# Optimization experiments

Measured on AMD Instinct MI355X. Metric: run time of the kernel, lower is better.

Reference implementation:

```python
import jax, jax.numpy as jnp
import numpy as np
from jax import lax

# CRF hyperparameters (init_kwargs)
MAX_ITER = 10
POS_W, POS_X_STD, POS_Y_STD = 3.0, 3.0, 3.0
BI_W, BI_X_STD, BI_Y_STD = 10.0, 80.0, 80.0
BI_R_STD, BI_G_STD, BI_B_STD = 13.0, 13.0, 13.0


def setup_inputs() -> dict:
    key = jax.random.key(0)
    k1, k2 = jax.random.split(key)
    U = jax.random.normal(k1, (1, 21, 96, 96), dtype=jnp.float32)      # unary energies
    I = jax.random.uniform(k2, (1, 3, 96, 96), dtype=jnp.float32) * 255.0  # RGB image 0..255
    return {"U": U, "I": I}


def _gauss1d(std):
    r = int(3.0 * std)
    x = jnp.arange(-r, r + 1, dtype=jnp.float32)
    return jnp.exp(-0.5 * (x / std) ** 2), r


def _spatial_raw(x, ky, kx, ry, rx):
    # x: [M, 1, H, W]; unnormalized separable Gaussian filter
    x = lax.conv_general_dilated(x, ky.reshape(1, 1, -1, 1), (1, 1), [(ry, ry), (0, 0)],
                                 dimension_numbers=("NCHW", "OIHW", "NCHW"))
    x = lax.conv_general_dilated(x, kx.reshape(1, 1, 1, -1), (1, 1), [(0, 0), (rx, rx)],
                                 dimension_numbers=("NCHW", "OIHW", "NCHW"))
    return x


def reference(U, I):
    B, L, H, W = U.shape
    N = H * W
    ky, ry = _gauss1d(POS_Y_STD)
    kx, rx = _gauss1d(POS_X_STD)

    # symmetric normalization for the spatial kernel: 1/sqrt(k * 1)
    nsp = lax.rsqrt(_spatial_raw(jnp.ones((1, 1, H, W), jnp.float32), ky, kx, ry, rx))  # [1,1,H,W]

    # bilateral kernel K[b, i, j] = exp(-0.5 ||f_i - f_j||^2) over 5-d features
    yy, xx = jnp.meshgrid(jnp.arange(H, dtype=jnp.float32), jnp.arange(W, dtype=jnp.float32), indexing="ij")
    pos = jnp.stack([xx.ravel() / BI_X_STD, yy.ravel() / BI_Y_STD], axis=-1)  # [N, 2]
    rgb_std = jnp.array([BI_R_STD, BI_G_STD, BI_B_STD], jnp.float32)
    col = I.reshape(B, 3, N).transpose(0, 2, 1) / rgb_std                     # [B, N, 3]
    feats = jnp.concatenate([jnp.broadcast_to(pos[None], (B, N, 2)), col], axis=-1)  # [B, N, 5]
    sq = jnp.sum(feats * feats, axis=-1)                                      # [B, N]
    D = sq[:, :, None] + sq[:, None, :] - 2.0 * jnp.einsum("bnf,bmf->bnm", feats, feats)
    K = jnp.exp(-0.5 * jnp.maximum(D, 0.0))                                   # [B, N, N]
    nbi = lax.rsqrt(jnp.sum(K, axis=-1, keepdims=True))                       # [B, N, 1]

    Q0 = jax.nn.softmax(-U, axis=1)

    def step(Q, _):
        Qf = Q.reshape(B * L, 1, H, W)
        sp_msg = POS_W * (nsp * _spatial_raw(nsp * Qf, ky, kx, ry, rx)).reshape(B, L, H, W)
        Qflat = Q.transpose(0, 2, 3, 1).reshape(B, N, L)
        bi = nbi * jnp.einsum("bnm,bml->bnl", K, nbi * Qflat)
        bi_msg = BI_W * bi.reshape(B, H, W, L).transpose(0, 3, 1, 2)
        # Potts compatibility (negative identity): agreeing mass raises the logit
        Qn = jax.nn.softmax(-U + sp_msg + bi_msg, axis=1)
        return Qn, None

    Q, _ = lax.scan(step, Q0, None, length=MAX_ITER)
    return Q
```

## Files before the change

### kernel.cpp

```cpp
#include <hip/hip_runtime.h>
#include <hip/hip_bf16.h>
#include <stddef.h>

#define HH 96
#define WW 96
#define NPIX 9216
#define LBL 21
#define LPAD 32
#define RAD 9
#define N_ITER 10
#define POS_W_C 3.0f
#define BI_W_C 10.0f
#define INV_XY (1.0f/80.0f)
#define INV_RGB (1.0f/13.0f)

#define JCH 16
#define JC (NPIX / JCH)
#define JTOT (NPIX / 32)
#define ITILE 64
#define NITB (NPIX / ITILE)
#define NSPB (LBL * 24)
#define KSPLIT 8
#define PSTR 24
#define QHALF (JTOT * 64 * 8)

typedef __bf16 bf16x8 __attribute__((ext_vector_type(8)));
typedef float  f32x4  __attribute__((ext_vector_type(4)));

__device__ const float GK[2 * RAD + 1] = {
    0.01110900f, 0.02856548f, 0.06572886f, 0.13533528f, 0.24935220f,
    0.41111229f, 0.60653066f, 0.80073740f, 0.94595947f, 1.00000000f,
    0.94595947f, 0.80073740f, 0.60653066f, 0.41111229f, 0.24935220f,
    0.13533528f, 0.06572886f, 0.02856548f, 0.01110900f
};

__device__ __forceinline__ unsigned short f2bf(float f) {
    unsigned u = __float_as_uint(f);
    unsigned r = (u + 0x7fffu + ((u >> 16) & 1u)) >> 16;
    return (unsigned short)r;
}
__device__ __forceinline__ float bf2f(unsigned short s) {
    return __uint_as_float(((unsigned)s) << 16);
}
__device__ __forceinline__ unsigned pk2bf(float a, float b) {
    __hip_bfloat162 h = __float22bfloat162_rn(make_float2(a, b));
    return *(unsigned*)&h;
}
__device__ __forceinline__ size_t qtidx(int p, int l) {
    size_t half = (l >> 4) ? (size_t)QHALF : 0;
    return half + ((((p >> 5) * 64 + ((p >> 3) & 3) * 16 + (l & 15)) << 3) + (p & 7));
}

__global__ void k_prep(const float* __restrict__ I,
                       float* __restrict__ fx, float* __restrict__ fy,
                       float* __restrict__ fr, float* __restrict__ fg,
                       float* __restrict__ fb, float* __restrict__ S,
                       float* __restrict__ nsp) {
    int n = blockIdx.x * 256 + threadIdx.x;
    if (n >= NPIX) return;
    int y = n / WW, x = n % WW;
    float vx = (float)x * INV_XY;
    float vy = (float)y * INV_XY;
    float vr = I[n] * INV_RGB;
    float vg = I[NPIX + n] * INV_RGB;
    float vb = I[2 * NPIX + n] * INV_RGB;
    fx[n] = vx; fy[n] = vy; fr[n] = vr; fg[n] = vg; fb[n] = vb;
    S[n] = -0.5f * (vx*vx + vy*vy + vr*vr + vg*vg + vb*vb);
    float sy = 0.f, sx = 0.f;
    #pragma unroll
    for (int d = -RAD; d <= RAD; ++d) {
        float g = GK[d + RAD];
        if ((unsigned)(y + d) < HH) sy += g;
        if ((unsigned)(x + d) < WW) sx += g;
    }
    nsp[n] = rsqrtf(sy * sx);
}

template <bool STORE>
__global__ void __launch_bounds__(256)
k_K(const float* __restrict__ fx, const float* __restrict__ fy,
    const float* __restrict__ fr, const float* __restrict__ fg,
    const float* __restrict__ fb, const float* __restrict__ S,
    float* __restrict__ RS, unsigned short* __restrict__ K) {
    int it = blockIdx.x >> 3;
    int part = blockIdx.x & 7;
    int tid = threadIdx.x;
    int m = tid & 15;
    int g = tid >> 4;
    int khs = g & 3;
    int ts = g >> 2;
    int i = it * 16 + m;
    float hx = fx[i], hy = fy[i], hr = fr[i], hg = fg[i], hb = fb[i];
    float ci = S[i];
    unsigned short* Kb = K + (size_t)it * JTOT * 512;
    float sum = 0.f;
    for (int pass = 0; pass < JTOT / (4 * KSPLIT); ++pass) {
        int jtile = part * (JTOT / KSPLIT) + pass * 4 + ts;
        int j = jtile * 32 + khs * 8;
        float4 x0 = *(const float4*)(fx + j), x1 = *(const float4*)(fx + j + 4);
        float4 y0 = *(const float4*)(fy + j), y1 = *(const float4*)(fy + j + 4);
        float4 r0 = *(const float4*)(fr + j), r1 = *(const float4*)(fr + j + 4);
        float4 g0 = *(const float4*)(fg + j), g1 = *(const float4*)(fg + j + 4);
        float4 b0 = *(const float4*)(fb + j), b1 = *(const float4*)(fb + j + 4);
        float4 s0 = *(const float4*)(S + j),  s1 = *(const float4*)(S + j + 4);
        float k0 = __expf(ci + s0.x + hx*x0.x + hy*y0.x + hr*r0.x + hg*g0.x + hb*b0.x);
        float k1 = __expf(ci + s0.y + hx*x0.y + hy*y0.y + hr*r0.y + hg*g0.y + hb*b0.y);
        float k2 = __expf(ci + s0.z + hx*x0.z + hy*y0.z + hr*r0.z + hg*g0.z + hb*b0.z);
        float k3 = __expf(ci + s0.w + hx*x0.w + hy*y0.w + hr*r0.w + hg*g0.w + hb*b0.w);
        float k4 = __expf(ci + s1.x + hx*x1.x + hy*y1.x + hr*r1.x + hg*g1.x + hb*b1.x);
        float k5 = __expf(ci + s1.y + hx*x1.y + hy*y1.y + hr*r1.y + hg*g1.y + hb*b1.y);
        float k6 = __expf(ci + s1.z + hx*x1.z + hy*y1.z + hr*r1.z + hg*g1.z + hb*b1.z);
        float k7 = __expf(ci + s1.w + hx*x1.w + hy*y1.w + hr*r1.w + hg*g1.w + hb*b1.w);
        sum += ((k0 + k1) + (k2 + k3)) + ((k4 + k5) + (k6 + k7));
        if (STORE) {
            uint4 u;
            u.x = pk2bf(k0, k1);
            u.y = pk2bf(k2, k3);
            u.z = pk2bf(k4, k5);
            u.w = pk2bf(k6, k7);
            *(uint4*)(Kb + (size_t)jtile * 512 + (tid & 63) * 8) = u;
        }
    }
    __shared__ float red[16][17];
    red[g][m] = sum;
    __syncthreads();
    if (tid < 16) {
        float tot = 0.f;
        #pragma unroll
        for (int q = 0; q < 16; ++q) tot += red[q][tid];
        RS[part * NPIX + it * 16 + tid] = tot;
    }
}

__global__ void k_q0(const float* __restrict__ U, const float* __restrict__ RS,
                     const float* __restrict__ nsp,
                     float* __restrict__ nbi, float* __restrict__ A,
                     unsigned short* __restrict__ Qt0, unsigned short* __restrict__ Qt1) {
    int n = blockIdx.x * 256 + threadIdx.x;
    if (n >= NPIX) return;
    float rs = 0.f;
    #pragma unroll
    for (int q = 0; q < KSPLIT; ++q) rs += RS[q * NPIX + n];
    float nb = rsqrtf(rs);
    nbi[n] = nb;
    float v[LBL];
    float mx = -1e30f;
    #pragma unroll
    for (int l = 0; l < LBL; ++l) { v[l] = -U[l * NPIX + n]; mx = fmaxf(mx, v[l]); }
    float s = 0.f;
    #pragma unroll
    for (int l = 0; l < LBL; ++l) { v[l] = __expf(v[l] - mx); s += v[l]; }
    float inv = 1.f / s;
    float ns = nsp[n];
    #pragma unroll
    for (int l = 0; l < LBL; ++l) {
        float q = v[l] * inv;
        A[l * NPIX + n] = ns * q;
        Qt0[qtidx(n, l)] = f2bf(nb * q);
    }
    #pragma unroll
    for (int l = LBL; l < LPAD; ++l) {
        Qt0[qtidx(n, l)] = 0;
        Qt1[qtidx(n, l)] = 0;
    }
}

__global__ void k_sp(const float* __restrict__ A, const float* __restrict__ nsp,
                     const float* __restrict__ U, float* __restrict__ SP) {
    __shared__ float ty[4 * WW];
    int l = blockIdx.x / 24;
    int y0 = (blockIdx.x % 24) * 4;
    int t = threadIdx.x;
    const float* Al = A + (size_t)l * NPIX;
    #pragma unroll
    for (int c = 0; c < 2; ++c) {
        int p = t + c * 256;
        if (p < 4 * WW) {
            int yy = p / WW, x = p % WW;
            int y = y0 + yy;
            float s = 0.f;
            #pragma unroll
            for (int d = -RAD; d <= RAD; ++d) {
                int yd = y + d;
                if ((unsigned)yd < HH) s += GK[d + RAD] * Al[yd * WW + x];
            }
            ty[p] = s;
        }
    }
    __syncthreads();
    #pragma unroll
    for (int c = 0; c < 2; ++c) {
        int p = t + c * 256;
        if (p < 4 * WW) {
            int yy = p / WW, x = p % WW;
            float s = 0.f;
            #pragma unroll
            for (int d = -RAD; d <= RAD; ++d) {
                int xd = x + d;
                if ((unsigned)xd < WW) s += GK[d + RAD] * ty[yy * WW + xd];
            }
            int pp = (y0 + yy) * WW + x;
            SP[(size_t)l * NPIX + pp] = POS_W_C * nsp[pp] * s - U[(size_t)l * NPIX + pp];
        }
    }
}

__global__ void __launch_bounds__(256, 8)
k_bi_fast(const unsigned short* __restrict__ K, const unsigned short* __restrict__ Qt,
          const float* __restrict__ A, const float* __restrict__ nsp,
          const float* __restrict__ U, float* __restrict__ SP,
          float* __restrict__ P) {
    int tid = threadIdx.x;
    int bid = blockIdx.x;

    __shared__ float ty[4 * WW];
    if (bid < NSPB) {
        int l = bid / 24;
        int y0b = (bid % 24) * 4;
        const float* Al = A + (size_t)l * NPIX;
        #pragma unroll
        for (int c = 0; c < 2; ++c) {
            int p = tid + c * 256;
            if (p < 4 * WW) {
                int yy = p / WW, x = p % WW;
                int y = y0b + yy;
                float s = 0.f;
                #pragma unroll
                for (int d = -RAD; d <= RAD; ++d) {
                    int yd = y + d;
                    if ((unsigned)yd < HH) s += GK[d + RAD] * Al[yd * WW + x];
                }
                ty[p] = s;
            }
        }
        __syncthreads();
        #pragma unroll
        for (int c = 0; c < 2; ++c) {
            int p = tid + c * 256;
            if (p < 4 * WW) {
                int yy = p / WW, x = p % WW;
                float s = 0.f;
                #pragma unroll
                for (int d = -RAD; d <= RAD; ++d) {
                    int xd = x + d;
                    if ((unsigned)xd < WW) s += GK[d + RAD] * ty[yy * WW + xd];
                }
                int pp = (y0b + yy) * WW + x;
                SP[(size_t)l * NPIX + pp] = POS_W_C * nsp[pp] * s - U[(size_t)l * NPIX + pp];
            }
        }
    }

    int jc  = bid / NITB;
    int itb = bid % NITB;
    int jtb = jc * (JC / 32);

    int lane = tid & 63;
    int wv = tid >> 6;
    int m  = lane & 15;
    int kh = lane >> 4;
    int it = itb * 4 + wv;

    const bf16x8* pa  = (const bf16x8*)K  + ((size_t)it * JTOT + jtb) * 64 + lane;
    const bf16x8* pb0 = (const bf16x8*)Qt + (size_t)jtb * 64 + lane;
    const bf16x8* pb1 = (const bf16x8*)Qt + (size_t)(QHALF / 8) + (size_t)jtb * 64 + lane;

    f32x4 acc0 = {0.f,0.f,0.f,0.f}, acc1 = {0.f,0.f,0.f,0.f};

    #pragma unroll 6
    for (int jt = 0; jt < JC / 32; ++jt) {
        bf16x8 a  = pa[jt * 64];
        bf16x8 b0 = pb0[jt * 64];
        bf16x8 b1 = pb1[jt * 64];
        acc0 = __builtin_amdgcn_mfma_f32_16x16x32_bf16(a, b0, acc0, 0, 0, 0);
        acc1 = __builtin_amdgcn_mfma_f32_16x16x32_bf16(a, b1, acc1, 0, 0, 0);
    }

    float* Pp = P + (size_t)jc * NPIX * PSTR;
    int i0 = it * 16 + kh * 4;
    #pragma unroll
    for (int r = 0; r < 4; ++r) {
        Pp[(size_t)(i0 + r) * PSTR + m] = acc0[r];
        if (m < 8) Pp[(size_t)(i0 + r) * PSTR + 16 + m] = acc1[r];
    }
}

__global__ void __launch_bounds__(256)
k_red(const float* __restrict__ P, const float* __restrict__ SP,
      const float* __restrict__ nbi, const float* __restrict__ nsp,
      float* __restrict__ Qo, float* __restrict__ Ao,
      unsigned short* __restrict__ Qto) {
    __shared__ float red[8][32][25];
    int tid = threadIdx.x;
    int p32 = tid & 31;
    int g = tid >> 5;
    int p = blockIdx.x * 32 + p32;

    float4 s[6] = {{0,0,0,0},{0,0,0,0},{0,0,0,0},{0,0,0,0},{0,0,0,0},{0,0,0,0}};
    #pragma unroll
    for (int jj = 0; jj < 2; ++jj) {
        int jcc = g * 2 + jj;
        const float4* pp = (const float4*)(P + ((size_t)jcc * NPIX + p) * PSTR);
        #pragma unroll
        for (int q = 0; q < 6; ++q) s[q] += pp[q];
    }
    #pragma unroll
    for (int q = 0; q < 6; ++q) {
        red[g][p32][4*q+0] = s[q].x;
        red[g][p32][4*q+1] = s[q].y;
        red[g][p32][4*q+2] = s[q].z;
        red[g][p32][4*q+3] = s[q].w;
    }
    __syncthreads();
    if (tid >= 32) return;

    float nb = nbi[p];
    float ns = nsp[p];
    float v[LBL];
    float mx = -1e30f;
    #pragma unroll
    for (int l = 0; l < LBL; ++l) {
        float bi = 0.f;
        #pragma unroll
        for (int q = 0; q < 8; ++q) bi += red[q][p32][l];
        v[l] = SP[l * NPIX + p] + BI_W_C * nb * bi;
        mx = fmaxf(mx, v[l]);
    }
    float ssum = 0.f;
    #pragma unroll
    for (int l = 0; l < LBL; ++l) { v[l] = __expf(v[l] - mx); ssum += v[l]; }
    float inv = 1.f / ssum;
    #pragma unroll
    for (int l = 0; l < LBL; ++l) {
        float q = v[l] * inv;
        Qo[l * NPIX + p] = q;
        Ao[l * NPIX + p] = ns * q;
        Qto[qtidx(p, l)] = f2bf(nb * q);
    }
}

__global__ void k_bi_slow(const float* __restrict__ fx, const float* __restrict__ fy,
                          const float* __restrict__ fr, const float* __restrict__ fg,
                          const float* __restrict__ fb,
                          const float* __restrict__ nbi, const unsigned short* __restrict__ Qt,
                          const float* __restrict__ SP, const float* __restrict__ nsp,
                          float* __restrict__ Qo, float* __restrict__ Ao,
                          unsigned short* __restrict__ Qto) {
    int t = threadIdx.x;
    int px = t & 15, st = t >> 4;
    int i = blockIdx.x * 16 + px;
    float xi = fx[i], yi = fy[i], ri = fr[i], gi = fg[i], bi = fb[i];
    float acc[LBL];
    #pragma unroll
    for (int l = 0; l < LBL; ++l) acc[l] = 0.f;
    int j0 = st * (NPIX / 16);
    for (int j = j0; j < j0 + NPIX / 16; ++j) {
        float dx = xi - fx[j], dy = yi - fy[j];
        float dr = ri - fr[j], dg = gi - fg[j], db = bi - fb[j];
        float D = dx*dx + dy*dy + dr*dr + dg*dg + db*db;
        float w = __expf(-0.5f * D);
        #pragma unroll
        for (int l = 0; l < LBL; ++l) acc[l] += w * bf2f(Qt[qtidx(j, l)]);
    }
    __shared__ float red[16][LBL];
    if (st == 0) {
        #pragma unroll
        for (int l = 0; l < LBL; ++l) red[px][l] = acc[l];
    }
    __syncthreads();
    for (int s = 1; s < 16; ++s) {
        if (st == s) {
            #pragma unroll
            for (int l = 0; l < LBL; ++l) red[px][l] += acc[l];
        }
        __syncthreads();
    }
    if (t < 16) {
        int i2 = blockIdx.x * 16 + t;
        float nb = nbi[i2];
        float ns = nsp[i2];
        float v[LBL];
        float mx = -1e30f;
        #pragma unroll
        for (int l = 0; l < LBL; ++l) {
            v[l] = SP[l * NPIX + i2] + BI_W_C * nb * red[t][l];
            mx = fmaxf(mx, v[l]);
        }
        float s = 0.f;
        #pragma unroll
        for (int l = 0; l < LBL; ++l) { v[l] = __expf(v[l] - mx); s += v[l]; }
        float inv = 1.f / s;
        #pragma unroll
        for (int l = 0; l < LBL; ++l) {
            float q = v[l] * inv;
            Qo[l * NPIX + i2] = q;
            Ao[l * NPIX + i2] = ns * q;
            Qto[qtidx(i2, l)] = f2bf(nb * q);
        }
    }
}

extern "C" void kernel_launch(void* const* d_in, const int* in_sizes, int n_in,
                              void* d_out, int out_size, void* d_ws, size_t ws_size,
                              hipStream_t stream) {
    const float* U = (const float*)d_in[0];
    const float* I = (const float*)d_in[1];

    char* w = (char*)d_ws;
    float* fx  = (float*)w;                 w += NPIX * sizeof(float);
    float* fy  = (float*)w;                 w += NPIX * sizeof(float);
    float* fr  = (float*)w;                 w += NPIX * sizeof(float);
    float* fg  = (float*)w;                 w += NPIX * sizeof(float);
    float* fb  = (float*)w;                 w += NPIX * sizeof(float);
    float* S   = (float*)w;                 w += NPIX * sizeof(float);
    float* nsp = (float*)w;                 w += NPIX * sizeof(float);
    float* nbi = (float*)w;                 w += NPIX * sizeof(float);
    float* RS  = (float*)w;                 w += (size_t)KSPLIT * NPIX * sizeof(float);
    float* A   = (float*)w;                 w += (size_t)LBL * NPIX * sizeof(float);
    float* SP  = (float*)w;                 w += (size_t)LBL * NPIX * sizeof(float);
    unsigned short* Qtb[2];
    Qtb[0] = (unsigned short*)w;            w += (size_t)2 * QHALF * sizeof(unsigned short);
    Qtb[1] = (unsigned short*)w;            w += (size_t)2 * QHALF * sizeof(unsigned short);
    float* P = (float*)w;                   w += (size_t)JCH * NPIX * PSTR * sizeof(float);
    unsigned short* K = (unsigned short*)w;
    size_t need = (size_t)(w - (char*)d_ws) + (size_t)NPIX * NPIX * sizeof(unsigned short);
    bool fast = (ws_size >= need);

    float* Qout = (float*)d_out;

    k_prep<<<(NPIX + 255) / 256, 256, 0, stream>>>(I, fx, fy, fr, fg, fb, S, nsp);
    if (fast) k_K<true ><<<(NPIX / 16) * KSPLIT, 256, 0, stream>>>(fx, fy, fr, fg, fb, S, RS, K);
    else      k_K<false><<<(NPIX / 16) * KSPLIT, 256, 0, stream>>>(fx, fy, fr, fg, fb, S, RS, nullptr);
    k_q0<<<(NPIX + 255) / 256, 256, 0, stream>>>(U, RS, nsp, nbi, A, Qtb[0], Qtb[1]);

    for (int t = 0; t < N_ITER; ++t) {
        const unsigned short* Qtin = Qtb[t & 1];
        unsigned short* Qtout = Qtb[(t + 1) & 1];
        if (fast) {
            k_bi_fast<<<NITB * JCH, 256, 0, stream>>>(K, Qtin, A, nsp, U, SP, P);
            k_red<<<NPIX / 32, 256, 0, stream>>>(P, SP, nbi, nsp, Qout, A, Qtout);
        } else {
            k_sp<<<NSPB, 256, 0, stream>>>(A, nsp, U, SP);
            k_bi_slow<<<NPIX / 16, 256, 0, stream>>>(fx, fy, fr, fg, fb, nbi, Qtin, SP, nsp, Qout, A, Qtout);
        }
    }
}
```

Baseline: 509.4 us.

## Compute two row tiles per wave in bilateral MFMA with A prefetch

Each wave in the bilateral matmul kernel now computes two 16-row output tiles instead of one. The ITILE doubles to 128, so each block covers twice as many rows and the grid halves. The Q operand fragments are loaded once per step and shared by both tiles, and the next step's K fragments are software-prefetched while the current MFMAs run. The aim is to cut Q loads and hide global-load latency on the K stream. In exchange, register use rises and launch bounds drop to 4 blocks per SM, which lowers occupancy.

```diff
diff --git a/kernel.cpp b/kernel.cpp
--- a/kernel.cpp
+++ b/kernel.cpp
@@ -17,7 +17,7 @@
 #define JCH 16
 #define JC (NPIX / JCH)
 #define JTOT (NPIX / 32)
-#define ITILE 64
+#define ITILE 128
 #define NITB (NPIX / ITILE)
 #define NSPB (LBL * 24)
 #define KSPLIT 8
@@ -205,7 +205,7 @@
     }
 }
 
-__global__ void __launch_bounds__(256, 8)
+__global__ void __launch_bounds__(256, 4)
 k_bi_fast(const unsigned short* __restrict__ K, const unsigned short* __restrict__ Qt,
           const float* __restrict__ A, const float* __restrict__ nsp,
           const float* __restrict__ U, float* __restrict__ SP,
@@ -259,29 +259,50 @@
     int wv = tid >> 6;
     int m  = lane & 15;
     int kh = lane >> 4;
-    int it = itb * 4 + wv;
-
-    const bf16x8* pa  = (const bf16x8*)K  + ((size_t)it * JTOT + jtb) * 64 + lane;
+
+    const bf16x8* pa0 = (const bf16x8*)K + ((size_t)(itb * 8 + wv)     * JTOT + jtb) * 64 + lane;
+    const bf16x8* pa1 = (const bf16x8*)K + ((size_t)(itb * 8 + 4 + wv) * JTOT + jtb) * 64 + lane;
     const bf16x8* pb0 = (const bf16x8*)Qt + (size_t)jtb * 64 + lane;
     const bf16x8* pb1 = (const bf16x8*)Qt + (size_t)(QHALF / 8) + (size_t)jtb * 64 + lane;
 
-    f32x4 acc0 = {0.f,0.f,0.f,0.f}, acc1 = {0.f,0.f,0.f,0.f};
-
-    #pragma unroll 6
-    for (int jt = 0; jt < JC / 32; ++jt) {
-        bf16x8 a  = pa[jt * 64];
+    f32x4 acc00 = {0.f,0.f,0.f,0.f}, acc01 = {0.f,0.f,0.f,0.f};
+    f32x4 acc10 = {0.f,0.f,0.f,0.f}, acc11 = {0.f,0.f,0.f,0.f};
+
+    bf16x8 a0c = pa0[0];
+    bf16x8 a1c = pa1[0];
+    #pragma unroll
+    for (int jt = 0; jt < JC / 32 - 1; ++jt) {
+        bf16x8 a0n = pa0[(jt + 1) * 64];
+        bf16x8 a1n = pa1[(jt + 1) * 64];
         bf16x8 b0 = pb0[jt * 64];
         bf16x8 b1 = pb1[jt * 64];
-        acc0 = __builtin_amdgcn_mfma_f32_16x16x32_bf16(a, b0, acc0, 0, 0, 0);
-        acc1 = __builtin_amdgcn_mfma_f32_16x16x32_bf16(a, b1, acc1, 0, 0, 0);
+        acc00 = __builtin_amdgcn_mfma_f32_16x16x32_bf16(a0c, b0, acc00, 0, 0, 0);
+        acc01 = __builtin_amdgcn_mfma_f32_16x16x32_bf16(a0c, b1, acc01, 0, 0, 0);
+        acc10 = __builtin_amdgcn_mfma_f32_16x16x32_bf16(a1c, b0, acc10, 0, 0, 0);
+        acc11 = __builtin_amdgcn_mfma_f32_16x16x32_bf16(a1c, b1, acc11, 0, 0, 0);
+        a0c = a0n; a1c = a1n;
+    }
+    {
+        int jt = JC / 32 - 1;
+        bf16x8 b0 = pb0[jt * 64];
+        bf16x8 b1 = pb1[jt * 64];
+        acc00 = __builtin_amdgcn_mfma_f32_16x16x32_bf16(a0c, b0, acc00, 0, 0, 0);
+        acc01 = __builtin_amdgcn_mfma_f32_16x16x32_bf16(a0c, b1, acc01, 0, 0, 0);
+        acc10 = __builtin_amdgcn_mfma_f32_16x16x32_bf16(a1c, b0, acc10, 0, 0, 0);
+        acc11 = __builtin_amdgcn_mfma_f32_16x16x32_bf16(a1c, b1, acc11, 0, 0, 0);
     }
 
     float* Pp = P + (size_t)jc * NPIX * PSTR;
-    int i0 = it * 16 + kh * 4;
+    int i0 = itb * 128 + wv * 16 + kh * 4;
+    int i1 = i0 + 64;
     #pragma unroll
     for (int r = 0; r < 4; ++r) {
-        Pp[(size_t)(i0 + r) * PSTR + m] = acc0[r];
-        if (m < 8) Pp[(size_t)(i0 + r) * PSTR + 16 + m] = acc1[r];
+        Pp[(size_t)(i0 + r) * PSTR + m] = acc00[r];
+        Pp[(size_t)(i1 + r) * PSTR + m] = acc10[r];
+        if (m < 8) {
+            Pp[(size_t)(i0 + r) * PSTR + 16 + m] = acc01[r];
+            Pp[(size_t)(i1 + r) * PSTR + 16 + m] = acc11[r];
+        }
     }
 }
 
```

After: 520.2 us. 1.02x slower.
